# Optimization experiments

Measured on AMD Instinct MI355X. Metric: run time of the kernel, lower is better.

## Reference

```python
import jax, jax.numpy as jnp
import numpy as np

EPS = 1e-8

def rms_norm(x, scale):
    # full RMSNorm over last dim (p < 0 branch): norm/sqrt(d)
    d = x.shape[-1]
    norm = jnp.linalg.norm(x, ord=2, axis=-1, keepdims=True)
    rms = norm * (d ** -0.5)
    return scale * (x / (rms + EPS))

def setup_inputs() -> dict:
    key = jax.random.key(0)
    ks = jax.random.split(key, 4)
    B, N, C, H = 2, 2048, 1024, 16
    hd = C // H
    x = jax.random.normal(ks[0], (B, N, C), dtype=jnp.float32)
    Wqkv = jax.random.normal(ks[1], (C, 3 * C), dtype=jnp.float32) * (C ** -0.5)
    Wproj = jax.random.normal(ks[2], (C, C), dtype=jnp.float32) * (C ** -0.5)
    bproj = jnp.zeros((C,), dtype=jnp.float32)
    q_scale = jnp.ones((hd,), dtype=jnp.float32)
    k_scale = jnp.ones((hd,), dtype=jnp.float32)
    return {"x": x, "Wqkv": Wqkv, "Wproj": Wproj, "bproj": bproj,
            "q_scale": q_scale, "k_scale": k_scale}

def reference(x, Wqkv, Wproj, bproj, q_scale, k_scale):
    B, N, C = x.shape
    H = 16
    hd = C // H
    scale = hd ** -0.5
    qkv = (x @ Wqkv).reshape(B, N, 3, H, hd)
    qkv = jnp.transpose(qkv, (2, 0, 3, 1, 4))  # t b h n c
    q, k, v = qkv[0], qkv[1], qkv[2]
    q = rms_norm(q, q_scale)
    k = rms_norm(k, k_scale)
    attn = jnp.einsum('bhnc,bhmc->bhnm', q, k) * scale
    attn = jax.nn.softmax(attn, axis=-1)
    out = jnp.einsum('bhnm,bhmc->bhnc', attn, v)
    out = jnp.transpose(out, (0, 2, 1, 3)).reshape(B, N, C)
    return out @ Wproj + bproj
```

## Files before the change

kernel.cpp:

```cpp
#include <hip/hip_runtime.h>


typedef _Float16 half_t;
typedef __attribute__((ext_vector_type(2))) __fp16 fp16x2;
typedef __attribute__((ext_vector_type(4))) _Float16 half4v;
typedef __attribute__((ext_vector_type(8))) _Float16 half8;
typedef __attribute__((ext_vector_type(4))) float f32x4;
typedef __attribute__((ext_vector_type(4))) unsigned uint4v;

#define DI __device__ __forceinline__

DI void gl_lds16(const void* g, void* l) {
    __builtin_amdgcn_global_load_lds((const __attribute__((address_space(1))) void*)g,
                                     (__attribute__((address_space(3))) void*)l, 16, 0, 0);
}

DI float exp2_fast(float x) {
    float r;
    asm("v_exp_f32 %0, %1" : "=v"(r) : "v"(x));
    return r;
}

DI void pl32_swap(unsigned& a, unsigned& b) {
    asm("v_permlane32_swap_b32 %0, %1" : "+v"(a), "+v"(b));
}
DI void pl16_swap(unsigned& a, unsigned& b) {
    asm("v_permlane16_swap_b32 %0, %1" : "+v"(a), "+v"(b));
}

DI unsigned pk_u32(float lo, float hi) {
    fp16x2 t = __builtin_amdgcn_cvt_pkrtz(lo, hi);
    return *(unsigned*)&t;
}

__global__ void prep_all(const float* __restrict__ x, const float* __restrict__ Wqkv,
                         const float* __restrict__ Wproj, half_t* __restrict__ xh,
                         half_t* __restrict__ wqt, half_t* __restrict__ wpt) {
    __shared__ float t[32][33];
    int bid = blockIdx.x;
    if (bid < 4096) {
        int i = (bid * 256 + threadIdx.x) * 4;
        float4 v = *(const float4*)(x + i);
        half4v o;
        o[0] = (half_t)v.x; o[1] = (half_t)v.y; o[2] = (half_t)v.z; o[3] = (half_t)v.w;
        *(half4v*)(xh + i) = o;
    } else if (bid < 4096 + 3072) {
        int i = bid - 4096;
        int c0 = (i % 96) * 32, r0 = (i / 96) * 32;
        int tx = threadIdx.x & 31, ty = threadIdx.x >> 5;
#pragma unroll
        for (int k = 0; k < 4; k++)
            t[ty + 8 * k][tx] = Wqkv[(size_t)(r0 + ty + 8 * k) * 3072 + c0 + tx];
        __syncthreads();
#pragma unroll
        for (int k = 0; k < 4; k++)
            wqt[(size_t)(c0 + ty + 8 * k) * 1024 + r0 + tx] = (half_t)t[tx][ty + 8 * k];
    } else {
        int i = bid - 4096 - 3072;
        int c0 = (i % 32) * 32, r0 = (i / 32) * 32;
        int tx = threadIdx.x & 31, ty = threadIdx.x >> 5;
#pragma unroll
        for (int k = 0; k < 4; k++)
            t[ty + 8 * k][tx] = Wproj[(size_t)(r0 + ty + 8 * k) * 1024 + c0 + tx];
        __syncthreads();
#pragma unroll
        for (int k = 0; k < 4; k++)
            wpt[(size_t)(c0 + ty + 8 * k) * 1024 + r0 + tx] = (half_t)t[tx][ty + 8 * k];
    }
}

__global__ __launch_bounds__(256, 4) void gemm_qkv(
    const half_t* __restrict__ A, const half_t* __restrict__ Bt,
    const float* __restrict__ qs, const float* __restrict__ ks,
    half_t* __restrict__ qh, half_t* __restrict__ kh, half_t* __restrict__ vth) {
    const int K = 1024;
    __shared__ __align__(16) half_t Al[2][128 * 32];
    __shared__ __align__(16) half_t Bl[2][128 * 32];
    int tid = threadIdx.x;
    int w = tid >> 6, l = tid & 63;
    int wr = w >> 1, wc = w & 1;
    int g = l >> 4, r = l & 15;
    int m0 = blockIdx.x * 128, n0 = blockIdx.y * 128;
    f32x4 acc[4][4] = {};

#define STAGE_QKV(kt, buf)                                                        \
    {                                                                             \
        _Pragma("unroll")                                                         \
        for (int p = 0; p < 2; p++) {                                             \
            int ci = p * 256 + tid;                                               \
            int row = ci >> 2, c = ci & 3, lc = c ^ ((row >> 1) & 3);             \
            gl_lds16(A + (size_t)(m0 + row) * K + (kt) * 32 + lc * 8,             \
                     &Al[buf][0] + ci * 8);                                       \
            gl_lds16(Bt + (size_t)(n0 + row) * K + (kt) * 32 + lc * 8,            \
                     &Bl[buf][0] + ci * 8);                                       \
        }                                                                         \
    }

    STAGE_QKV(0, 0);
    __syncthreads();
    int cur = 0;
    for (int kt = 0; kt < 32; kt++) {
        if (kt < 31) STAGE_QKV(kt + 1, cur ^ 1);
        half8 af[4], bf[4];
#pragma unroll
        for (int i = 0; i < 4; i++) {
            int row = wr * 64 + i * 16 + r;
            af[i] = *(const half8*)(&Al[cur][0] + row * 32 + ((g ^ ((row >> 1) & 3)) << 3));
            int rowb = wc * 64 + i * 16 + r;
            bf[i] = *(const half8*)(&Bl[cur][0] + rowb * 32 + ((g ^ ((rowb >> 1) & 3)) << 3));
        }
#pragma unroll
        for (int i = 0; i < 4; i++)
#pragma unroll
            for (int j = 0; j < 4; j++)
                acc[i][j] = __builtin_amdgcn_mfma_f32_16x16x32_f16(af[i], bf[j], acc[i][j], 0, 0, 0);
        __syncthreads();
        cur ^= 1;
    }

    int tsec = n0 >> 10;
    if (tsec == 2) {
#pragma unroll
        for (int i = 0; i < 4; i++)
#pragma unroll
            for (int j = 0; j < 4; j++) {
                int gcol = n0 + wc * 64 + j * 16 + r;
                int h = (gcol >> 6) & 15;
                int f = gcol & 63;
                int growb = m0 + wr * 64 + i * 16 + g * 4;
                int b = growb >> 11;
                int n = growb & 2047;
                half4v pv;
#pragma unroll
                for (int rr = 0; rr < 4; rr++) pv[rr] = (half_t)acc[i][j][rr];
                *(half4v*)(vth + ((size_t)(b * 16 + h) * 64 + f) * 2048 + n) = pv;
            }
    } else {
        const float* sc = (tsec == 0) ? qs : ks;
        half_t* dst = (tsec == 0) ? qh : kh;
        float extra = (tsec == 0) ? (0.125f * 1.44269504f) : 1.0f;
        float scv[4];
#pragma unroll
        for (int j = 0; j < 4; j++) scv[j] = sc[j * 16 + r];
#pragma unroll
        for (int i = 0; i < 4; i++)
#pragma unroll
            for (int rr = 0; rr < 4; rr++) {
                float ss = 0.f;
#pragma unroll
                for (int j = 0; j < 4; j++) ss += acc[i][j][rr] * acc[i][j][rr];
#pragma unroll
                for (int d = 1; d < 16; d <<= 1) ss += __shfl_xor(ss, d, 64);
                float inv = extra / (sqrtf(ss) * 0.125f + 1e-8f);
                int grow = m0 + wr * 64 + i * 16 + g * 4 + rr;
                int b = grow >> 11;
                int n = grow & 2047;
#pragma unroll
                for (int j = 0; j < 4; j++) {
                    int gcol = n0 + wc * 64 + j * 16 + r;
                    int h = (gcol >> 6) & 15;
                    int f = gcol & 63;
                    dst[((size_t)(b * 16 + h) * 2048 + n) * 64 + f] =
                        (half_t)(acc[i][j][rr] * inv * scv[j]);
                }
            }
    }
}

__global__ __launch_bounds__(512, 8) void attn(
    const half_t* __restrict__ qh, const half_t* __restrict__ kh,
    const half_t* __restrict__ vth, half_t* __restrict__ aoh) {
    int bh = blockIdx.y;
    int q0 = blockIdx.x * 64;
    int tid = threadIdx.x, w = tid >> 6, l = tid & 63, g = l >> 4, r = l & 15;
    int hf = w >> 2, qs = w & 3, lt = tid & 255;

    const half_t* Qp = qh + (size_t)bh * 2048 * 64;
    const half_t* Kp = kh + (size_t)bh * 2048 * 64 + (size_t)hf * 1024 * 64;
    const half_t* Vp = vth + (size_t)bh * 64 * 2048 + hf * 1024;

    __shared__ __align__(16) char smem[32768];
    half_t* Kb[2] = {(half_t*)(smem + hf * 8192), (half_t*)(smem + hf * 8192 + 4096)};
    half_t* Vb[2] = {(half_t*)(smem + 16384 + hf * 8192), (half_t*)(smem + 16384 + hf * 8192 + 4096)};

    int krow = lt >> 3, kc = lt & 7, klc = kc ^ (krow & 7);
    const half_t* kst = Kp + (size_t)krow * 64 + klc * 8;
    int vrow = lt >> 2, vc = lt & 3, vlc = vc ^ ((vrow >> 1) & 3);
    const half_t* vst = Vp + (size_t)vrow * 2048 + vlc * 8;

    int koff[4], voff[4];
#pragma unroll
    for (int ks = 0; ks < 2; ks++)
#pragma unroll
        for (int tt = 0; tt < 2; tt++) {
            int row = tt * 16 + r;
            koff[ks * 2 + tt] = row * 64 + (((ks * 4 + g) ^ (row & 7)) << 3);
        }
#pragma unroll
    for (int cf = 0; cf < 4; cf++) {
        int row = cf * 16 + r;
        voff[cf] = row * 32 + ((g ^ ((row >> 1) & 3)) << 3);
    }

    half8 qf[2];
#pragma unroll
    for (int ks = 0; ks < 2; ks++)
        qf[ks] = *(const half8*)(Qp + (size_t)(q0 + qs * 16 + r) * 64 + ks * 32 + g * 8);

    f32x4 o[4] = {};
    float m = -1e30f, lsum = 0.f;

    gl_lds16(kst, Kb[0] + lt * 8);
    gl_lds16(vst, Vb[0] + lt * 8);
    __syncthreads();

#define ATTN_TILE(BUF, T)                                                          \
    {                                                                              \
        if ((T) < 31) {                                                            \
            gl_lds16(kst + ((T) + 1) * 2048, Kb[(BUF) ^ 1] + lt * 8);              \
            gl_lds16(vst + ((T) + 1) * 32, Vb[(BUF) ^ 1] + lt * 8);                \
        }                                                                          \
        const half_t* Kc = Kb[BUF];                                                \
        const half_t* Vc = Vb[BUF];                                                \
        f32x4 s[2] = {};                                                           \
        _Pragma("unroll")                                                          \
        for (int ks = 0; ks < 2; ks++)                                             \
            _Pragma("unroll")                                                      \
            for (int tt = 0; tt < 2; tt++) {                                       \
                half8 kf = *(const half8*)(Kc + koff[ks * 2 + tt]);                \
                s[tt] = __builtin_amdgcn_mfma_f32_16x16x32_f16(kf, qf[ks], s[tt], 0, 0, 0); \
            }                                                                      \
        float thr = m + 11.0f;                                                     \
        bool ok = true;                                                            \
        _Pragma("unroll")                                                          \
        for (int tt = 0; tt < 2; tt++)                                             \
            _Pragma("unroll")                                                      \
            for (int e = 0; e < 4; e++) ok = ok && (s[tt][e] <= thr);              \
        if (!__all(ok)) {                                                          \
            float mx = fmaxf(fmaxf(s[0][0], s[0][1]), fmaxf(s[0][2], s[0][3]));    \
            mx = fmaxf(mx, fmaxf(fmaxf(s[1][0], s[1][1]), fmaxf(s[1][2], s[1][3]))); \
            mx = fmaxf(mx, __shfl_xor(mx, 16, 64));                                \
            mx = fmaxf(mx, __shfl_xor(mx, 32, 64));                                \
            float mn = fmaxf(m, mx);                                               \
            float fac = exp2_fast(m - mn);                                         \
            lsum *= fac;                                                           \
            _Pragma("unroll")                                                      \
            for (int cf = 0; cf < 4; cf++) {                                       \
                o[cf][0] *= fac; o[cf][1] *= fac; o[cf][2] *= fac; o[cf][3] *= fac; \
            }                                                                      \
            m = mn;                                                                \
        }                                                                          \
        _Pragma("unroll")                                                          \
        for (int tt = 0; tt < 2; tt++)                                             \
            _Pragma("unroll")                                                      \
            for (int e = 0; e < 4; e++) {                                          \
                float p = exp2_fast(s[tt][e] - m);                                 \
                s[tt][e] = p;                                                      \
                lsum += p;                                                         \
            }                                                                      \
        unsigned b0 = pk_u32(s[0][0], s[0][1]);                                    \
        unsigned b1 = pk_u32(s[0][2], s[0][3]);                                    \
        unsigned b2 = pk_u32(s[1][0], s[1][1]);                                    \
        unsigned b3 = pk_u32(s[1][2], s[1][3]);                                    \
        pl32_swap(b0, b2); pl16_swap(b0, b2);                                      \
        pl32_swap(b1, b3); pl16_swap(b1, b3);                                      \
        uint4v pw; pw[0] = b0; pw[1] = b1; pw[2] = b2; pw[3] = b3;                 \
        half8 pf = *(half8*)&pw;                                                   \
        _Pragma("unroll")                                                          \
        for (int cf = 0; cf < 4; cf++) {                                           \
            half8 vf = *(const half8*)(Vc + voff[cf]);                             \
            o[cf] = __builtin_amdgcn_mfma_f32_16x16x32_f16(vf, pf, o[cf], 0, 0, 0); \
        }                                                                          \
        __syncthreads();                                                           \
    }

    for (int t = 0; t < 32; t += 2) {
        ATTN_TILE(0, t);
        ATTN_TILE(1, t + 1);
    }

    lsum += __shfl_xor(lsum, 16, 64);
    lsum += __shfl_xor(lsum, 32, 64);

    float* mo = (float*)smem;
    float* mml = (float*)(smem + 17408);
    int q2 = qs * 16 + r;
    if (hf) {
#pragma unroll
        for (int cf = 0; cf < 4; cf++)
            *(f32x4*)(mo + q2 * 68 + cf * 16 + g * 4) = o[cf];
        if (l < 16) {
            mml[q2 * 2] = m;
            mml[q2 * 2 + 1] = lsum;
        }
    }
    __syncthreads();
    if (!hf) {
        float m1 = mml[q2 * 2], ls1 = mml[q2 * 2 + 1];
        float M = fmaxf(m, m1);
        float w0 = exp2_fast(m - M), w1 = exp2_fast(m1 - M);
        float inv = 1.0f / (w0 * lsum + w1 * ls1);
        w0 *= inv; w1 *= inv;
        int n = q0 + q2;
        int b = bh >> 4, h = bh & 15;
#pragma unroll
        for (int cf = 0; cf < 4; cf++) {
            f32x4 o1 = *(const f32x4*)(mo + q2 * 68 + cf * 16 + g * 4);
            half4v ov;
#pragma unroll
            for (int e = 0; e < 4; e++) ov[e] = (half_t)(o[cf][e] * w0 + o1[e] * w1);
            *(half4v*)(aoh + ((size_t)b * 2048 + n) * 1024 + h * 64 + cf * 16 + g * 4) = ov;
        }
    }
}

__global__ __launch_bounds__(256) void gemm_proj(
    const half_t* __restrict__ A, const half_t* __restrict__ Bt,
    const float* __restrict__ bias, float* __restrict__ out) {
    const int K = 1024;
    __shared__ __align__(16) half_t Al[128 * 64];
    __shared__ __align__(16) half_t Bl[128 * 64];
    int tid = threadIdx.x, w = tid >> 6, l = tid & 63;
    int wr = w >> 1, wc = w & 1, g = l >> 4, r = l & 15;
    int m0 = blockIdx.x * 128, n0 = blockIdx.y * 128;
    f32x4 acc[4][4] = {};

    for (int k0 = 0; k0 < K; k0 += 64) {
#pragma unroll
        for (int p = 0; p < 4; p++) {
            int ci = (p * 4 + w) * 64 + l;
            int row = ci >> 3, c = ci & 7;
            int lc = c ^ (row & 7);
            gl_lds16(A + (size_t)(m0 + row) * K + k0 + lc * 8, Al + (p * 4 + w) * 512);
            gl_lds16(Bt + (size_t)(n0 + row) * K + k0 + lc * 8, Bl + (p * 4 + w) * 512);
        }
        __syncthreads();
#pragma unroll
        for (int ks = 0; ks < 2; ks++) {
            half8 af[4], bf[4];
#pragma unroll
            for (int i = 0; i < 4; i++) {
                int row = wr * 64 + i * 16 + r;
                af[i] = *(const half8*)(Al + row * 64 + (((4 * ks + g) ^ (row & 7)) << 3));
                int rowb = wc * 64 + i * 16 + r;
                bf[i] = *(const half8*)(Bl + rowb * 64 + (((4 * ks + g) ^ (rowb & 7)) << 3));
            }
#pragma unroll
            for (int i = 0; i < 4; i++)
#pragma unroll
                for (int j = 0; j < 4; j++)
                    acc[i][j] = __builtin_amdgcn_mfma_f32_16x16x32_f16(af[i], bf[j], acc[i][j], 0, 0, 0);
        }
        __syncthreads();
    }

#pragma unroll
    for (int i = 0; i < 4; i++)
#pragma unroll
        for (int j = 0; j < 4; j++) {
            int gcol = n0 + wc * 64 + j * 16 + r;
            float bv = bias[gcol];
#pragma unroll
            for (int rr = 0; rr < 4; rr++) {
                int grow = m0 + wr * 64 + i * 16 + g * 4 + rr;
                out[(size_t)grow * 1024 + gcol] = acc[i][j][rr] + bv;
            }
        }
}

extern "C" void kernel_launch(void* const* d_in, const int* in_sizes, int n_in,
                              void* d_out, int out_size, void* d_ws, size_t ws_size,
                              hipStream_t stream) {
    const float* x = (const float*)d_in[0];
    const float* Wqkv = (const float*)d_in[1];
    const float* Wproj = (const float*)d_in[2];
    const float* bproj = (const float*)d_in[3];
    const float* qscale = (const float*)d_in[4];
    const float* kscale = (const float*)d_in[5];
    float* out = (float*)d_out;

    char* ws = (char*)d_ws;
    half_t* xh  = (half_t*)(ws + 0);
    half_t* wqt = (half_t*)(ws + 8388608);
    half_t* wpt = (half_t*)(ws + 14680064);
    half_t* qh  = (half_t*)(ws + 16777216);
    half_t* kh  = (half_t*)(ws + 25165824);
    half_t* vth = (half_t*)(ws + 33554432);
    half_t* aoh = (half_t*)(ws + 41943040);

    prep_all<<<8192, 256, 0, stream>>>(x, Wqkv, Wproj, xh, wqt, wpt);
    gemm_qkv<<<dim3(32, 24), 256, 0, stream>>>(xh, wqt, qscale, kscale, qh, kh, vth);
    attn<<<dim3(32, 32), 512, 0, stream>>>(qh, kh, vth, aoh);
    gemm_proj<<<dim3(32, 8), 256, 0, stream>>>(aoh, wpt, bproj, out);
}
```

Baseline: 124.9 us.

## Double-buffer proj GEMM LDS loads and halve M tile for more blocks

The output projection GEMM now uses a 64x128 tile with K-step 32 and two LDS buffers. The next K slice is prefetched while the current one is computed, and the swizzle is adjusted to the 32-wide rows. The grid doubles to 512 blocks so more workgroups run across the CUs, and launch bounds request 4 waves per SIMD. In exchange there are more syncs per K, less reuse of B per block, and more redundant B loads.

```diff
diff --git a/kernel.cpp b/kernel.cpp
--- a/kernel.cpp
+++ b/kernel.cpp
@@ -314,55 +314,68 @@
     }
 }
 
-__global__ __launch_bounds__(256) void gemm_proj(
+__global__ __launch_bounds__(256, 4) void gemm_proj(
     const half_t* __restrict__ A, const half_t* __restrict__ Bt,
     const float* __restrict__ bias, float* __restrict__ out) {
     const int K = 1024;
-    __shared__ __align__(16) half_t Al[128 * 64];
-    __shared__ __align__(16) half_t Bl[128 * 64];
+    __shared__ __align__(16) half_t Al[2][64 * 32];
+    __shared__ __align__(16) half_t Bl[2][128 * 32];
     int tid = threadIdx.x, w = tid >> 6, l = tid & 63;
     int wr = w >> 1, wc = w & 1, g = l >> 4, r = l & 15;
-    int m0 = blockIdx.x * 128, n0 = blockIdx.y * 128;
-    f32x4 acc[4][4] = {};
-
-    for (int k0 = 0; k0 < K; k0 += 64) {
-#pragma unroll
-        for (int p = 0; p < 4; p++) {
-            int ci = (p * 4 + w) * 64 + l;
-            int row = ci >> 3, c = ci & 7;
-            int lc = c ^ (row & 7);
-            gl_lds16(A + (size_t)(m0 + row) * K + k0 + lc * 8, Al + (p * 4 + w) * 512);
-            gl_lds16(Bt + (size_t)(n0 + row) * K + k0 + lc * 8, Bl + (p * 4 + w) * 512);
-        }
+    int m0 = blockIdx.x * 64, n0 = blockIdx.y * 128;
+    f32x4 acc[2][4] = {};
+
+#define STAGE_PROJ(kt, buf)                                                       \
+    {                                                                             \
+        {                                                                         \
+            int ci = tid;                                                         \
+            int row = ci >> 2, c = ci & 3, lc = c ^ ((row >> 1) & 3);             \
+            gl_lds16(A + (size_t)(m0 + row) * K + (kt) * 32 + lc * 8,             \
+                     &Al[buf][0] + ci * 8);                                       \
+        }                                                                         \
+        _Pragma("unroll")                                                         \
+        for (int p = 0; p < 2; p++) {                                             \
+            int ci = p * 256 + tid;                                               \
+            int row = ci >> 2, c = ci & 3, lc = c ^ ((row >> 1) & 3);             \
+            gl_lds16(Bt + (size_t)(n0 + row) * K + (kt) * 32 + lc * 8,            \
+                     &Bl[buf][0] + ci * 8);                                       \
+        }                                                                         \
+    }
+
+    STAGE_PROJ(0, 0);
+    __syncthreads();
+    int cur = 0;
+    for (int kt = 0; kt < 32; kt++) {
+        if (kt < 31) STAGE_PROJ(kt + 1, cur ^ 1);
+        half8 af[2], bf[4];
+#pragma unroll
+        for (int i = 0; i < 2; i++) {
+            int row = wr * 32 + i * 16 + r;
+            af[i] = *(const half8*)(&Al[cur][0] + row * 32 + ((g ^ ((row >> 1) & 3)) << 3));
+        }
+#pragma unroll
+        for (int j = 0; j < 4; j++) {
+            int rowb = wc * 64 + j * 16 + r;
+            bf[j] = *(const half8*)(&Bl[cur][0] + rowb * 32 + ((g ^ ((rowb >> 1) & 3)) << 3));
+        }
+#pragma unroll
+        for (int i = 0; i < 2; i++)
+#pragma unroll
+            for (int j = 0; j < 4; j++)
+                acc[i][j] = __builtin_amdgcn_mfma_f32_16x16x32_f16(af[i], bf[j], acc[i][j], 0, 0, 0);
         __syncthreads();
-#pragma unroll
-        for (int ks = 0; ks < 2; ks++) {
-            half8 af[4], bf[4];
-#pragma unroll
-            for (int i = 0; i < 4; i++) {
-                int row = wr * 64 + i * 16 + r;
-                af[i] = *(const half8*)(Al + row * 64 + (((4 * ks + g) ^ (row & 7)) << 3));
-                int rowb = wc * 64 + i * 16 + r;
-                bf[i] = *(const half8*)(Bl + rowb * 64 + (((4 * ks + g) ^ (rowb & 7)) << 3));
-            }
-#pragma unroll
-            for (int i = 0; i < 4; i++)
-#pragma unroll
-                for (int j = 0; j < 4; j++)
-                    acc[i][j] = __builtin_amdgcn_mfma_f32_16x16x32_f16(af[i], bf[j], acc[i][j], 0, 0, 0);
-        }
-        __syncthreads();
-    }
-
-#pragma unroll
-    for (int i = 0; i < 4; i++)
+        cur ^= 1;
+    }
+
+#pragma unroll
+    for (int i = 0; i < 2; i++)
 #pragma unroll
         for (int j = 0; j < 4; j++) {
             int gcol = n0 + wc * 64 + j * 16 + r;
             float bv = bias[gcol];
 #pragma unroll
             for (int rr = 0; rr < 4; rr++) {
-                int grow = m0 + wr * 64 + i * 16 + g * 4 + rr;
+                int grow = m0 + wr * 32 + i * 16 + g * 4 + rr;
                 out[(size_t)grow * 1024 + gcol] = acc[i][j][rr] + bv;
             }
         }
@@ -391,5 +404,5 @@
     prep_all<<<8192, 256, 0, stream>>>(x, Wqkv, Wproj, xh, wqt, wpt);
     gemm_qkv<<<dim3(32, 24), 256, 0, stream>>>(xh, wqt, qscale, kscale, qh, kh, vth);
     attn<<<dim3(32, 32), 512, 0, stream>>>(qh, kh, vth, aoh);
-    gemm_proj<<<dim3(32, 8), 256, 0, stream>>>(aoh, wpt, bproj, out);
-}
+    gemm_proj<<<dim3(64, 8), 256, 0, stream>>>(aoh, wpt, bproj, out);
+}
```

New measurement: 123.6 us (median of 3 runs). About the same (-1.0%).
